# Optimization experiments

Hardware: AMD Instinct MI355X
Metric: run time of the kernel (lower is better)

## Reference

```python
import jax, jax.numpy as jnp
import numpy as np

N = 50000; E = 800000; F_IN = 128; H = 16; G = 256
DIMS = [F_IN, H, 2 * H, 4 * H, 4 * H, 8 * H]
EPS = 1e-5


def setup_inputs() -> dict:
    key = jax.random.key(0)
    ks = iter(jax.random.split(key, 40))
    inp = {}
    inp["x"] = jax.random.normal(next(ks), (N, F_IN), dtype=jnp.float32)
    inp["edge_index"] = jax.random.randint(next(ks), (2, E), 0, N, dtype=jnp.int32)
    inp["edge_weight"] = jax.random.uniform(next(ks), (E,), dtype=jnp.float32)
    inp["batch"] = jnp.sort(jax.random.randint(next(ks), (N,), 0, G, dtype=jnp.int32))
    for i in range(5):
        din, dout = DIMS[i], DIMS[i + 1]
        inp[f"W{i+1}"] = jax.random.normal(next(ks), (din, dout), dtype=jnp.float32) / np.sqrt(din).astype(np.float32)
        inp[f"b{i+1}"] = jnp.zeros((dout,), jnp.float32)
        inp[f"g{i+1}"] = jnp.ones((dout,), jnp.float32)
        inp[f"bt{i+1}"] = jnp.zeros((dout,), jnp.float32)
    inp["fc1_w"] = jax.random.normal(next(ks), (8 * H, 4 * H), dtype=jnp.float32) / np.sqrt(8 * H).astype(np.float32)
    inp["fc1_b"] = jnp.zeros((4 * H,), jnp.float32)
    inp["fc2_w"] = jax.random.normal(next(ks), (4 * H, 1), dtype=jnp.float32) / np.sqrt(4 * H).astype(np.float32)
    inp["fc2_b"] = jnp.zeros((1,), jnp.float32)
    return inp


def _gcn_norm(edge_index, edge_weight, n):
    # PyG GCNConv: add self-loops (weight 1), symmetric deg^-1/2 normalization.
    loop = jnp.arange(n, dtype=edge_index.dtype)
    row = jnp.concatenate([edge_index[0], loop])  # source
    col = jnp.concatenate([edge_index[1], loop])  # target
    w = jnp.concatenate([edge_weight, jnp.ones((n,), edge_weight.dtype)])
    deg = jax.ops.segment_sum(w, col, num_segments=n)
    dis = jnp.where(deg > 0, jax.lax.rsqrt(jnp.maximum(deg, 1e-12)), 0.0)
    return row, col, dis[row] * w * dis[col]


def _bn(h, g, b):
    # BatchNorm1d, training-mode batch statistics (biased variance, eps=1e-5)
    mu = h.mean(0)
    v = h.var(0)
    return g * (h - mu) * jax.lax.rsqrt(v + EPS) + b


def reference(x, edge_index, edge_weight, batch,
              W1, b1, g1, bt1, W2, b2, g2, bt2, W3, b3, g3, bt3,
              W4, b4, g4, bt4, W5, b5, g5, bt5,
              fc1_w, fc1_b, fc2_w, fc2_b):
    n = x.shape[0]
    row, col, norm = _gcn_norm(edge_index, edge_weight, n)

    def conv(h, W, b):
        m = h @ W                                   # [N, dout] dense transform
        agg = jax.ops.segment_sum(m[row] * norm[:, None], col, num_segments=n)
        return agg + b

    h = _bn(jax.nn.relu(conv(x, W1, b1)), g1, bt1)
    h = _bn(jax.nn.relu(conv(h, W2, b2)), g2, bt2)
    h = _bn(jax.nn.relu(conv(h, W3, b3)), g3, bt3)
    h = jax.nn.relu(_bn(conv(h, W4, b4), g4, bt4))   # layer4: conv->bn->relu
    h = _bn(conv(h, W5, b5), g5, bt5)                # layer5: conv->bn
    pooled = jax.ops.segment_sum(h, batch, num_segments=G)  # global_add_pool -> [G, 8H]
    p = jax.nn.relu(pooled)
    p = jax.nn.relu(p @ fc1_w + fc1_b)
    # dropout is identity in eval mode
    return (p @ fc2_w + fc2_b).reshape(-1)          # [G]
```

## Files before the change

### kernel.cpp

```cpp
#include <hip/hip_runtime.h>
#include <stdint.h>

#define NN 50000
#define NE 800000
#define NG 256
#define NBUCKET 16
#define PARTSZ (NBUCKET * 256)

#define NBKT 391
#define ABLK 391
#define ASLICE 2048
#define BCAP 2560

__device__ __forceinline__ float bf2f(unsigned short u) {
    return __uint_as_float(((unsigned)u) << 16);
}
__device__ __forceinline__ unsigned short f2bf(float f) {
    unsigned b = __float_as_uint(f);
    return (unsigned short)((b + 0x7FFF + ((b >> 16) & 1)) >> 16);
}

__global__ void kA1(const int* __restrict__ col, int* __restrict__ bb, float* part, int e) {
    __shared__ int cnt[NBKT];
    for (int j = threadIdx.x; j < NBKT; j += 256) cnt[j] = 0;
    for (int i = blockIdx.x * 256 + threadIdx.x; i < 5 * PARTSZ; i += ABLK * 256) part[i] = 0.f;
    __syncthreads();
    int start = blockIdx.x * ASLICE;
    int end = min(start + ASLICE, e);
    for (int i = start + threadIdx.x; i < end; i += 256)
        atomicAdd(&cnt[col[i] >> 7], 1);
    __syncthreads();
    for (int j = threadIdx.x; j < NBKT; j += 256) bb[blockIdx.x * NBKT + j] = cnt[j];
}

__global__ void kA2a(int* __restrict__ bb, int* __restrict__ totals) {
    __shared__ int v[ABLK];
    int k = blockIdx.x;
    for (int b = threadIdx.x; b < ABLK; b += 256) v[b] = bb[b * NBKT + k];
    __syncthreads();
    if (threadIdx.x == 0) {
        int run = 0;
        for (int b = 0; b < ABLK; ++b) { int t = v[b]; v[b] = run; run += t; }
        totals[k] = run;
    }
    __syncthreads();
    for (int b = threadIdx.x; b < ABLK; b += 256) bb[b * NBKT + k] = v[b];
}

__global__ void kA2b(const int* __restrict__ totals, int* __restrict__ bucketbase) {
    __shared__ int v[NBKT];
    for (int j = threadIdx.x; j < NBKT; j += 256) v[j] = totals[j];
    __syncthreads();
    if (threadIdx.x == 0) {
        int run = 0;
        for (int k = 0; k < NBKT; ++k) { int t = v[k]; v[k] = run; run += t; }
        bucketbase[NBKT] = run;
    }
    __syncthreads();
    for (int j = threadIdx.x; j < NBKT; j += 256) bucketbase[j] = v[j];
}

__global__ void kA3g(const int* __restrict__ row, const int* __restrict__ col,
                     const float* __restrict__ ew, const int* __restrict__ bb,
                     const int* __restrict__ bucketbase, int2* __restrict__ staging,
                     const float* __restrict__ x, const float* __restrict__ W0,
                     float* __restrict__ m1, int e, int n) {
    __shared__ int cur[NBKT];
    __shared__ float Wl[128 * 16];
    int tid = threadIdx.x;
    if ((int)blockIdx.x < ABLK) {
        for (int j = tid; j < NBKT; j += 256)
            cur[j] = bucketbase[j] + bb[blockIdx.x * NBKT + j];
        __syncthreads();
        int start = blockIdx.x * ASLICE;
        int end = min(start + ASLICE, e);
        for (int i = start + tid; i < end; i += 256) {
            int c = col[i];
            int p = atomicAdd(&cur[c >> 7], 1);
            staging[p] = make_int2(row[i] | ((c & 127) << 16), __float_as_int(ew[i]));
        }
        return;
    }
    int bid = (int)blockIdx.x - ABLK;
    for (int i = tid; i < 128 * 16 / 4; i += 256)
        ((float4*)Wl)[i] = ((const float4*)W0)[i];
    __syncthreads();
    int jq = tid % 4, group = tid / 4;
    int node0 = (bid * 64 + group) * 2;
    const float4* h4 = (const float4*)x;
    int hb[2]; bool val[2];
#pragma unroll
    for (int i = 0; i < 2; ++i) {
        int nd = node0 + i;
        val[i] = nd < n;
        hb[i] = (val[i] ? nd : n - 1) * 32;
    }
    float4 acc[2];
    acc[0] = {0,0,0,0}; acc[1] = {0,0,0,0};
#pragma unroll 4
    for (int k4 = 0; k4 < 32; ++k4) {
        const float* wb = &Wl[(k4 * 4) * 16 + jq * 4];
        float4 w0 = *(const float4*)(wb);
        float4 w1 = *(const float4*)(wb + 16);
        float4 w2 = *(const float4*)(wb + 32);
        float4 w3 = *(const float4*)(wb + 48);
#pragma unroll
        for (int i = 0; i < 2; ++i) {
            float4 hv = h4[hb[i] + k4];
            acc[i].x += hv.x*w0.x + hv.y*w1.x + hv.z*w2.x + hv.w*w3.x;
            acc[i].y += hv.x*w0.y + hv.y*w1.y + hv.z*w2.y + hv.w*w3.y;
            acc[i].z += hv.x*w0.z + hv.y*w1.z + hv.z*w2.z + hv.w*w3.z;
            acc[i].w += hv.x*w0.w + hv.y*w1.w + hv.z*w2.w + hv.w*w3.w;
        }
    }
#pragma unroll
    for (int i = 0; i < 2; ++i)
        if (val[i]) ((float4*)m1)[(node0 + i) * 4 + jq] = acc[i];
}

__global__ void __launch_bounds__(256) kB(const int* __restrict__ bucketbase,
                                          const int2* __restrict__ staging,
                                          int2* __restrict__ csr, int* __restrict__ ptr,
                                          float* __restrict__ dis, int n) {
    __shared__ int2 st[BCAP];
    __shared__ int2 outb[BCAP];
    __shared__ int hist[129];
    __shared__ int cur[128];
    int k = blockIdx.x, t = threadIdx.x;
    int base = bucketbase[k], cnt = bucketbase[k + 1] - base;
    int node0 = k << 7;
    int ncov = min(128, n - node0);
    if (t < 129) hist[t] = 0;
    __syncthreads();
    if (cnt <= BCAP) {
        for (int i = t; i < cnt; i += 256) {
            int2 v = staging[base + i];
            st[i] = v;
            atomicAdd(&hist[v.x >> 16], 1);
        }
        __syncthreads();
        if (t == 0) {
            int run = 0;
            for (int j = 0; j < 128; ++j) { int h = hist[j]; hist[j] = run; run += h; }
            hist[128] = run;
        }
        __syncthreads();
        if (t < 128) cur[t] = hist[t];
        if (t < ncov) ptr[node0 + t] = base + hist[t];
        __syncthreads();
        for (int i = t; i < cnt; i += 256) {
            int2 v = st[i];
            int j = v.x >> 16;
            int p = atomicAdd(&cur[j], 1);
            outb[p] = make_int2(v.x & 0xFFFF, v.y);
        }
        __syncthreads();
        for (int i = t; i < cnt; i += 256) csr[base + i] = outb[i];
        if (t < ncov) {
            float s = 1.f;
            int a = hist[t], b2 = hist[t + 1];
            for (int p = a; p < b2; ++p) s += __int_as_float(outb[p].y);
            dis[node0 + t] = rsqrtf(s);
        }
    } else {
        for (int i = t; i < cnt; i += 256) atomicAdd(&hist[staging[base + i].x >> 16], 1);
        __syncthreads();
        if (t == 0) {
            int run = 0;
            for (int j = 0; j < 128; ++j) { int h = hist[j]; hist[j] = run; run += h; }
            hist[128] = run;
        }
        __syncthreads();
        if (t < 128) cur[t] = hist[t];
        if (t < ncov) ptr[node0 + t] = base + hist[t];
        __syncthreads();
        for (int i = t; i < cnt; i += 256) {
            int2 v = staging[base + i];
            int j = v.x >> 16;
            int p = atomicAdd(&cur[j], 1);
            csr[base + p] = make_int2(v.x & 0xFFFF, v.y);
        }
        __threadfence_block();
        __syncthreads();
        if (t < ncov) {
            float s = 1.f;
            int a = hist[t], b2 = hist[t + 1];
            for (int p = a; p < b2; ++p) s += __int_as_float(csr[base + p].y);
            dis[node0 + t] = rsqrtf(s);
        }
    }
    if (k == gridDim.x - 1 && t == 0) ptr[n] = bucketbase[NBKT];
}

__global__ void k_l1gather(const float* __restrict__ src, const int* __restrict__ ptr,
                           int2* __restrict__ csr, const float* __restrict__ dis,
                           const float* __restrict__ bias, float* __restrict__ partOut,
                           float* __restrict__ out, int n) {
    __shared__ float ls[16], lq[16];
    int tid = threadIdx.x;
    if (tid < 16) { ls[tid] = 0.f; lq[tid] = 0.f; }
    __syncthreads();
    int t = blockIdx.x * 256 + tid;
    int node = t >> 2;
    int l4 = t & 3;
    bool valid = node < n;
    int nc = valid ? node : n - 1;
    const float4* s4 = (const float4*)src;
    float dc = dis[nc];
    float w0 = dc * dc;
    float4 v = s4[nc * 4 + l4];
    float4 acc = { w0 * v.x, w0 * v.y, w0 * v.z, w0 * v.w };
    int p0 = ptr[nc], p1 = ptr[nc + 1];
    int p = p0;
    for (; p + 4 <= p1; p += 4) {
        int2 c0 = csr[p], c1 = csr[p+1], c2 = csr[p+2], c3 = csr[p+3];
        float e0 = dis[c0.x] * __int_as_float(c0.y) * dc;
        float e1 = dis[c1.x] * __int_as_float(c1.y) * dc;
        float e2 = dis[c2.x] * __int_as_float(c2.y) * dc;
        float e3 = dis[c3.x] * __int_as_float(c3.y) * dc;
        float4 u0 = s4[c0.x * 4 + l4];
        float4 u1 = s4[c1.x * 4 + l4];
        float4 u2 = s4[c2.x * 4 + l4];
        float4 u3 = s4[c3.x * 4 + l4];
        acc.x += e0*u0.x + e1*u1.x + e2*u2.x + e3*u3.x;
        acc.y += e0*u0.y + e1*u1.y + e2*u2.y + e3*u3.y;
        acc.z += e0*u0.z + e1*u1.z + e2*u2.z + e3*u3.z;
        acc.w += e0*u0.w + e1*u1.w + e2*u2.w + e3*u3.w;
        if (l4 == 0) {
            csr[p]   = make_int2(c0.x, __float_as_int(e0));
            csr[p+1] = make_int2(c1.x, __float_as_int(e1));
            csr[p+2] = make_int2(c2.x, __float_as_int(e2));
            csr[p+3] = make_int2(c3.x, __float_as_int(e3));
        }
    }
    for (; p < p1; ++p) {
        int2 ce = csr[p];
        float w = dis[ce.x] * __int_as_float(ce.y) * dc;
        float4 u = s4[ce.x * 4 + l4];
        acc.x += w*u.x; acc.y += w*u.y; acc.z += w*u.z; acc.w += w*u.w;
        if (l4 == 0) csr[p] = make_int2(ce.x, __float_as_int(w));
    }
    float4 b = ((const float4*)bias)[l4];
    acc.x = fmaxf(acc.x + b.x, 0.f);
    acc.y = fmaxf(acc.y + b.y, 0.f);
    acc.z = fmaxf(acc.z + b.z, 0.f);
    acc.w = fmaxf(acc.w + b.w, 0.f);
    if (valid) ((float4*)out)[nc * 4 + l4] = acc;
    float s0 = valid ? acc.x : 0.f, s1 = valid ? acc.y : 0.f;
    float s2 = valid ? acc.z : 0.f, s3 = valid ? acc.w : 0.f;
    float q0 = s0*s0, q1 = s1*s1, q2 = s2*s2, q3 = s3*s3;
    for (int off = 4; off < 64; off <<= 1) {
        s0 += __shfl_down(s0, off, 64); s1 += __shfl_down(s1, off, 64);
        s2 += __shfl_down(s2, off, 64); s3 += __shfl_down(s3, off, 64);
        q0 += __shfl_down(q0, off, 64); q1 += __shfl_down(q1, off, 64);
        q2 += __shfl_down(q2, off, 64); q3 += __shfl_down(q3, off, 64);
    }
    int lane = tid & 63;
    if (lane < 4) {
        atomicAdd(&ls[4*lane+0], s0); atomicAdd(&ls[4*lane+1], s1);
        atomicAdd(&ls[4*lane+2], s2); atomicAdd(&ls[4*lane+3], s3);
        atomicAdd(&lq[4*lane+0], q0); atomicAdd(&lq[4*lane+1], q1);
        atomicAdd(&lq[4*lane+2], q2); atomicAdd(&lq[4*lane+3], q3);
    }
    __syncthreads();
    int bkt = (blockIdx.x & (NBUCKET - 1)) * 256;
    if (tid < 16) {
        atomicAdd(&partOut[bkt + tid], ls[tid]);
        atomicAdd(&partOut[bkt + 128 + tid], lq[tid]);
    }
}

template <int D, int BF16>
__device__ __forceinline__ float4 load_row(const void* src, int node, int l4) {
    if (BF16) {
        const unsigned short* sb = (const unsigned short*)src;
        ushort4 r = *(const ushort4*)(sb + (size_t)node * D + (l4 << 2));
        float4 f;
        f.x = bf2f(r.x); f.y = bf2f(r.y); f.z = bf2f(r.z); f.w = bf2f(r.w);
        return f;
    } else {
        const float4* s4 = (const float4*)src;
        return s4[(size_t)node * (D / 4) + l4];
    }
}

template <int DIN, int DOUT, int EP, int POSTAFF, int PREAFF, int RELU,
          int BF16IN, int BF16OUT, int NPB>
__global__ void __launch_bounds__(256) k_fused(
        const void* __restrict__ src, const int* __restrict__ ptr,
        const int2* __restrict__ csr, const float* __restrict__ dis,
        const float* __restrict__ partIn, const float* __restrict__ gmv,
        const float* __restrict__ btv, const float* __restrict__ W,
        const float* __restrict__ bias, float* __restrict__ partOut,
        void* __restrict__ out, int n) {
    const int TPN1 = DIN / 4, LPN = TPN1 * EP, GN1 = 256 / LPN;
    const int TPN2 = DOUT / 4, G2 = 256 / TPN2;
    const int HS = DIN + 4;
    __shared__ float Wl[DIN * DOUT];
    __shared__ float hrow[NPB * HS];
    __shared__ float scs[DIN], shs[DIN];
    __shared__ float ls[DOUT], lq[DOUT];
    int tid = threadIdx.x;
    for (int i = tid; i < DIN * DOUT / 4; i += 256)
        ((float4*)Wl)[i] = ((const float4*)W)[i];
    if (tid < DIN) {
        float s = 0.f, q = 0.f;
#pragma unroll
        for (int b2 = 0; b2 < NBUCKET; ++b2) {
            s += partIn[b2 * 256 + tid];
            q += partIn[b2 * 256 + 128 + tid];
        }
        float mu = s / (float)n;
        float var = q / (float)n - mu * mu;
        float a = gmv[tid] * rsqrtf(var + 1e-5f);
        scs[tid] = a;
        shs[tid] = btv[tid] - mu * a;
    }
    if (tid < DOUT) { ls[tid] = 0.f; lq[tid] = 0.f; }
    __syncthreads();

    int nodebase = blockIdx.x * NPB;
    {
        int grp = tid / LPN, r = tid % LPN;
        int e0 = r / TPN1, l4 = r % TPN1;
        float4 sc = ((const float4*)scs)[l4];
        float4 sh = ((const float4*)shs)[l4];
#pragma unroll
        for (int pass = 0; pass < NPB / GN1; ++pass) {
            int nl = pass * GN1 + grp;
            int node = nodebase + nl;
            int nc = node < n ? node : n - 1;
            float4 acc = {0.f, 0.f, 0.f, 0.f};
            float sumw = 0.f;
            if (e0 == 0) {
                float d = dis[nc];
                float w0 = d * d;
                float4 v = load_row<DIN, BF16IN>(src, nc, l4);
                if (PREAFF) {
                    v.x = fmaxf(sc.x*v.x+sh.x, 0.f); v.y = fmaxf(sc.y*v.y+sh.y, 0.f);
                    v.z = fmaxf(sc.z*v.z+sh.z, 0.f); v.w = fmaxf(sc.w*v.w+sh.w, 0.f);
                }
                acc.x = w0*v.x; acc.y = w0*v.y; acc.z = w0*v.z; acc.w = w0*v.w;
                sumw = w0;
            }
            int p0 = ptr[nc], p1 = ptr[nc + 1];
            int p = p0 + e0;
            for (; p + 3 * EP < p1; p += 4 * EP) {
                int2 c0 = csr[p], c1 = csr[p + EP], c2 = csr[p + 2*EP], c3 = csr[p + 3*EP];
                float e0w = __int_as_float(c0.y), e1w = __int_as_float(c1.y);
                float e2w = __int_as_float(c2.y), e3w = __int_as_float(c3.y);
                float4 u0 = load_row<DIN, BF16IN>(src, c0.x, l4);
                float4 u1 = load_row<DIN, BF16IN>(src, c1.x, l4);
                float4 u2 = load_row<DIN, BF16IN>(src, c2.x, l4);
                float4 u3 = load_row<DIN, BF16IN>(src, c3.x, l4);
                if (PREAFF) {
                    u0.x = fmaxf(sc.x*u0.x+sh.x,0.f); u0.y = fmaxf(sc.y*u0.y+sh.y,0.f);
                    u0.z = fmaxf(sc.z*u0.z+sh.z,0.f); u0.w = fmaxf(sc.w*u0.w+sh.w,0.f);
                    u1.x = fmaxf(sc.x*u1.x+sh.x,0.f); u1.y = fmaxf(sc.y*u1.y+sh.y,0.f);
                    u1.z = fmaxf(sc.z*u1.z+sh.z,0.f); u1.w = fmaxf(sc.w*u1.w+sh.w,0.f);
                    u2.x = fmaxf(sc.x*u2.x+sh.x,0.f); u2.y = fmaxf(sc.y*u2.y+sh.y,0.f);
                    u2.z = fmaxf(sc.z*u2.z+sh.z,0.f); u2.w = fmaxf(sc.w*u2.w+sh.w,0.f);
                    u3.x = fmaxf(sc.x*u3.x+sh.x,0.f); u3.y = fmaxf(sc.y*u3.y+sh.y,0.f);
                    u3.z = fmaxf(sc.z*u3.z+sh.z,0.f); u3.w = fmaxf(sc.w*u3.w+sh.w,0.f);
                }
                acc.x += e0w*u0.x + e1w*u1.x + e2w*u2.x + e3w*u3.x;
                acc.y += e0w*u0.y + e1w*u1.y + e2w*u2.y + e3w*u3.y;
                acc.z += e0w*u0.z + e1w*u1.z + e2w*u2.z + e3w*u3.z;
                acc.w += e0w*u0.w + e1w*u1.w + e2w*u2.w + e3w*u3.w;
                if (POSTAFF) sumw += e0w + e1w + e2w + e3w;
            }
            for (; p < p1; p += EP) {
                int2 ce = csr[p];
                float w = __int_as_float(ce.y);
                float4 u = load_row<DIN, BF16IN>(src, ce.x, l4);
                if (PREAFF) {
                    u.x = fmaxf(sc.x*u.x+sh.x,0.f); u.y = fmaxf(sc.y*u.y+sh.y,0.f);
                    u.z = fmaxf(sc.z*u.z+sh.z,0.f); u.w = fmaxf(sc.w*u.w+sh.w,0.f);
                }
                acc.x += w*u.x; acc.y += w*u.y; acc.z += w*u.z; acc.w += w*u.w;
                if (POSTAFF) sumw += w;
            }
#pragma unroll
            for (int off = TPN1; off < LPN; off <<= 1) {
                acc.x += __shfl_xor(acc.x, off, 64);
                acc.y += __shfl_xor(acc.y, off, 64);
                acc.z += __shfl_xor(acc.z, off, 64);
                acc.w += __shfl_xor(acc.w, off, 64);
                if (POSTAFF) sumw += __shfl_xor(sumw, off, 64);
            }
            if (POSTAFF) {
                acc.x = sc.x * acc.x + sh.x * sumw;
                acc.y = sc.y * acc.y + sh.y * sumw;
                acc.z = sc.z * acc.z + sh.z * sumw;
                acc.w = sc.w * acc.w + sh.w * sumw;
            }
            if (e0 == 0) *(float4*)&hrow[nl * HS + (l4 << 2)] = acc;
        }
    }
    __syncthreads();
    {
        int jq = tid % TPN2, g2 = tid / TPN2;
        float4 bv = ((const float4*)bias)[jq];
        float4 sv = {0,0,0,0}, qv = {0,0,0,0};
        for (int nl = g2; nl < NPB; nl += G2) {
            int node = nodebase + nl;
            bool valid = node < n;
            float4 a = {0.f, 0.f, 0.f, 0.f};
#pragma unroll
            for (int k4 = 0; k4 < DIN / 4; ++k4) {
                float4 hv = *(const float4*)&hrow[nl * HS + (k4 << 2)];
                const float* wb = &Wl[(k4 * 4) * DOUT + jq * 4];
// ... 16 lines not shown
                    ushort4 o;
                    o.x = f2bf(a.x); o.y = f2bf(a.y); o.z = f2bf(a.z); o.w = f2bf(a.w);
                    *(ushort4*)((unsigned short*)out + (size_t)node * DOUT + (jq << 2)) = o;
                } else {
                    ((float4*)out)[(size_t)node * TPN2 + jq] = a;
                }
                sv.x += a.x; sv.y += a.y; sv.z += a.z; sv.w += a.w;
                qv.x += a.x*a.x; qv.y += a.y*a.y; qv.z += a.z*a.z; qv.w += a.w*a.w;
            }
        }
        for (int off = TPN2; off < 64; off <<= 1) {
            sv.x += __shfl_down(sv.x, off, 64); sv.y += __shfl_down(sv.y, off, 64);
            sv.z += __shfl_down(sv.z, off, 64); sv.w += __shfl_down(sv.w, off, 64);
            qv.x += __shfl_down(qv.x, off, 64); qv.y += __shfl_down(qv.y, off, 64);
            qv.z += __shfl_down(qv.z, off, 64); qv.w += __shfl_down(qv.w, off, 64);
        }
        int lane = tid & 63;
        if (lane < TPN2) {
            atomicAdd(&ls[4*lane+0], sv.x); atomicAdd(&ls[4*lane+1], sv.y);
            atomicAdd(&ls[4*lane+2], sv.z); atomicAdd(&ls[4*lane+3], sv.w);
            atomicAdd(&lq[4*lane+0], qv.x); atomicAdd(&lq[4*lane+1], qv.y);
            atomicAdd(&lq[4*lane+2], qv.z); atomicAdd(&lq[4*lane+3], qv.w);
        }
        __syncthreads();
        int bkt = (blockIdx.x & (NBUCKET - 1)) * 256;
        if (tid < DOUT) {
            atomicAdd(&partOut[bkt + tid], ls[tid]);
            atomicAdd(&partOut[bkt + 128 + tid], lq[tid]);
        }
    }
}

template <int D, int POSTAFF, int PREAFF>
__global__ void k_sgather(const unsigned short* __restrict__ src, const int* __restrict__ ptr,
                          const int2* __restrict__ csr, const float* __restrict__ dis,
                          const float* __restrict__ partIn, const float* __restrict__ gmv,
                          const float* __restrict__ btv, float* __restrict__ out, int n) {
    const int TPN = D / 4, EP = 4, LPN = TPN * EP;
    __shared__ float scs[D], shs[D];
    int tid = threadIdx.x;
    if (tid < D) {
        float s = 0.f, q = 0.f;
#pragma unroll
        for (int b2 = 0; b2 < NBUCKET; ++b2) {
            s += partIn[b2 * 256 + tid];
            q += partIn[b2 * 256 + 128 + tid];
        }
        float mu = s / (float)n;
        float var = q / (float)n - mu * mu;
        float a = gmv[tid] * rsqrtf(var + 1e-5f);
        scs[tid] = a;
        shs[tid] = btv[tid] - mu * a;
    }
    __syncthreads();
    int t = blockIdx.x * 256 + tid;
    int node = t / LPN;
    int r = t - node * LPN;
    int e0 = r / TPN;
    int l4 = r - e0 * TPN;
    bool valid = node < n;
    int nc = valid ? node : n - 1;
    float4 sc = ((const float4*)scs)[l4];
    float4 sh = ((const float4*)shs)[l4];
    float4 acc = {0.f, 0.f, 0.f, 0.f};
    float sumw = 0.f;
    if (e0 == 0) {
        float d = dis[nc];
        float w0 = d * d;
        float4 v = load_row<D, 1>(src, nc, l4);
        if (PREAFF) {
            v.x = fmaxf(sc.x*v.x+sh.x, 0.f); v.y = fmaxf(sc.y*v.y+sh.y, 0.f);
            v.z = fmaxf(sc.z*v.z+sh.z, 0.f); v.w = fmaxf(sc.w*v.w+sh.w, 0.f);
        }
        acc.x = w0*v.x; acc.y = w0*v.y; acc.z = w0*v.z; acc.w = w0*v.w;
        sumw = w0;
    }
    int p0 = ptr[nc], p1 = ptr[nc + 1];
    int p = p0 + e0;
    for (; p + 3 * EP < p1; p += 4 * EP) {
        int2 c0 = csr[p], c1 = csr[p + EP], c2 = csr[p + 2*EP], c3 = csr[p + 3*EP];
        float e0w = __int_as_float(c0.y), e1w = __int_as_float(c1.y);
        float e2w = __int_as_float(c2.y), e3w = __int_as_float(c3.y);
        float4 u0 = load_row<D, 1>(src, c0.x, l4);
        float4 u1 = load_row<D, 1>(src, c1.x, l4);
        float4 u2 = load_row<D, 1>(src, c2.x, l4);
        float4 u3 = load_row<D, 1>(src, c3.x, l4);
        if (PREAFF) {
            u0.x = fmaxf(sc.x*u0.x+sh.x,0.f); u0.y = fmaxf(sc.y*u0.y+sh.y,0.f);
            u0.z = fmaxf(sc.z*u0.z+sh.z,0.f); u0.w = fmaxf(sc.w*u0.w+sh.w,0.f);
            u1.x = fmaxf(sc.x*u1.x+sh.x,0.f); u1.y = fmaxf(sc.y*u1.y+sh.y,0.f);
            u1.z = fmaxf(sc.z*u1.z+sh.z,0.f); u1.w = fmaxf(sc.w*u1.w+sh.w,0.f);
            u2.x = fmaxf(sc.x*u2.x+sh.x,0.f); u2.y = fmaxf(sc.y*u2.y+sh.y,0.f);
            u2.z = fmaxf(sc.z*u2.z+sh.z,0.f); u2.w = fmaxf(sc.w*u2.w+sh.w,0.f);
            u3.x = fmaxf(sc.x*u3.x+sh.x,0.f); u3.y = fmaxf(sc.y*u3.y+sh.y,0.f);
            u3.z = fmaxf(sc.z*u3.z+sh.z,0.f); u3.w = fmaxf(sc.w*u3.w+sh.w,0.f);
        }
        acc.x += e0w*u0.x + e1w*u1.x + e2w*u2.x + e3w*u3.x;
        acc.y += e0w*u0.y + e1w*u1.y + e2w*u2.y + e3w*u3.y;
        acc.z += e0w*u0.z + e1w*u1.z + e2w*u2.z + e3w*u3.z;
        acc.w += e0w*u0.w + e1w*u1.w + e2w*u2.w + e3w*u3.w;
        if (POSTAFF) sumw += e0w + e1w + e2w + e3w;
    }
    for (; p < p1; p += EP) {
        int2 ce = csr[p];
        float w = __int_as_float(ce.y);
        float4 u = load_row<D, 1>(src, ce.x, l4);
        if (PREAFF) {
            u.x = fmaxf(sc.x*u.x+sh.x,0.f); u.y = fmaxf(sc.y*u.y+sh.y,0.f);
            u.z = fmaxf(sc.z*u.z+sh.z,0.f); u.w = fmaxf(sc.w*u.w+sh.w,0.f);
        }
        acc.x += w*u.x; acc.y += w*u.y; acc.z += w*u.z; acc.w += w*u.w;
        if (POSTAFF) sumw += w;
    }
#pragma unroll
    for (int off = TPN; off < LPN; off <<= 1) {
        acc.x += __shfl_xor(acc.x, off, 64);
        acc.y += __shfl_xor(acc.y, off, 64);
        acc.z += __shfl_xor(acc.z, off, 64);
        acc.w += __shfl_xor(acc.w, off, 64);
        if (POSTAFF) sumw += __shfl_xor(sumw, off, 64);
    }
    if (POSTAFF) {
        acc.x = sc.x * acc.x + sh.x * sumw;
        acc.y = sc.y * acc.y + sh.y * sumw;
        acc.z = sc.z * acc.z + sh.z * sumw;
        acc.w = sc.w * acc.w + sh.w * sumw;
    }
    if (valid && e0 == 0) ((float4*)out)[nc * TPN + l4] = acc;
}

template <int DIN, int DOUT, int RELU, int BF16OUT>
__global__ void k_sgemm(const float* __restrict__ h, const float* __restrict__ W,
                        const float* __restrict__ bias, float* __restrict__ partOut,
                        void* __restrict__ m, int n) {
    const int TPN = DOUT / 4, GPB = 256 / TPN, NPT = 4;
    __shared__ float Wl[DIN * DOUT];
    __shared__ float ls[DOUT], lq[DOUT];
    int tid = threadIdx.x;
    for (int i = tid; i < DIN * DOUT / 4; i += 256)
        ((float4*)Wl)[i] = ((const float4*)W)[i];
    if (tid < DOUT) { ls[tid] = 0.f; lq[tid] = 0.f; }
    __syncthreads();

    int jq = tid % TPN;
    int group = tid / TPN;
    int node0 = (blockIdx.x * GPB + group) * NPT;
    const float4* h4 = (const float4*)h;
    int hb[NPT]; bool val[NPT];
#pragma unroll
    for (int i = 0; i < NPT; ++i) {
        int nd = node0 + i;
        val[i] = nd < n;
        hb[i] = (val[i] ? nd : n - 1) * (DIN / 4);
    }
    float4 acc[NPT];
#pragma unroll
    for (int i = 0; i < NPT; ++i) acc[i] = {0.f, 0.f, 0.f, 0.f};
#pragma unroll 4
    for (int k4 = 0; k4 < DIN / 4; ++k4) {
        const float* wb = &Wl[(k4 * 4) * DOUT + jq * 4];
        float4 w0 = *(const float4*)(wb);
// ... 99 lines not shown
        for (int k = 0; k < 128; ++k) v1 += pl[k] * fc1w[k * 64 + tid];
        v1 = fmaxf(v1, 0.f);
        float v = v1 * fc2w[tid];
        for (int off = 32; off > 0; off >>= 1) v += __shfl_down(v, off, 64);
        if (tid == 0) out[g] = v + fc2b[0];
    }
}

extern "C" void kernel_launch(void* const* d_in, const int* in_sizes, int n_in,
                              void* d_out, int out_size, void* d_ws, size_t ws_size,
                              hipStream_t stream) {
    const float* x     = (const float*)d_in[0];
    const int*   ei    = (const int*)d_in[1];
    const float* ew    = (const float*)d_in[2];
    const int*   batch = (const int*)d_in[3];
    const float *W[5], *b[5], *gm[5], *bt[5];
    for (int i = 0; i < 5; ++i) {
        W[i]  = (const float*)d_in[4 + 4 * i];
        b[i]  = (const float*)d_in[5 + 4 * i];
        gm[i] = (const float*)d_in[6 + 4 * i];
        bt[i] = (const float*)d_in[7 + 4 * i];
    }
    const float* fc1w = (const float*)d_in[24];
    const float* fc1b = (const float*)d_in[25];
    const float* fc2w = (const float*)d_in[26];
    const float* fc2b = (const float*)d_in[27];
    float* out = (float*)d_out;

    char* wsb = (char*)d_ws;
    float* dis    = (float*)wsb;  wsb += sizeof(float) * NN;
    int*   ptr    = (int*)wsb;    wsb += sizeof(int) * (NN + 4);
    int*   bb     = (int*)wsb;    wsb += sizeof(int) * ABLK * NBKT;
    int*   totals = (int*)wsb;    wsb += sizeof(int) * (NBKT + 1);
    int*   bbase  = (int*)wsb;    wsb += sizeof(int) * (NBKT + 3);
    wsb = (char*)(((uintptr_t)wsb + 15) & ~(uintptr_t)15);
    int2*  staging= (int2*)wsb;   wsb += sizeof(int2) * NE;
    int2*  csr    = (int2*)wsb;   wsb += sizeof(int2) * NE;
    float* part   = (float*)wsb;  wsb += sizeof(float) * 5 * PARTSZ;
    unsigned short* bufB1 = (unsigned short*)wsb;  wsb += sizeof(unsigned short) * (size_t)NN * 64;
    unsigned short* bufB2 = (unsigned short*)wsb;  wsb += sizeof(unsigned short) * (size_t)NN * 64;
    float* buf1   = (float*)wsb;  wsb += sizeof(float) * (size_t)NN * 64;
    float* buf2   = (float*)wsb;  wsb += sizeof(float) * (size_t)NN * 128;

    const int* row = ei;
    const int* col = ei + NE;
    const int B = 256;
    const int NBF = (NN + 15) / 16;
    const int GB1 = (NN + 127) / 128;

    kA1<<<ABLK, B, 0, stream>>>(col, bb, part, NE);
    kA2a<<<NBKT, B, 0, stream>>>(bb, totals);
    kA2b<<<1, B, 0, stream>>>(totals, bbase);
    kA3g<<<ABLK + GB1, B, 0, stream>>>(row, col, ew, bb, bbase, staging, x, W[0], buf1, NE, NN);
    kB<<<NBKT, B, 0, stream>>>(bbase, staging, csr, ptr, dis, NN);

    k_l1gather<<<(NN * 4 + 255) / 256, B, 0, stream>>>(buf1, ptr, csr, dis,
                                                       b[0], part + 0 * PARTSZ, buf2, NN);

    k_fused<16, 32, 4, 1, 0, 1, 0, 1, 16><<<NBF, B, 0, stream>>>(
        buf2, ptr, csr, dis, part + 0 * PARTSZ, gm[0], bt[0],
        W[1], b[1], part + 1 * PARTSZ, bufB1, NN);

    k_sgather<32, 1, 0><<<(int)(((long)NN * 32 + 255) / 256), B, 0, stream>>>(
        bufB1, ptr, csr, dis, part + 1 * PARTSZ, gm[1], bt[1], buf1, NN);
    k_sgemm<32, 64, 1, 1><<<(NN + 63) / 64, B, 0, stream>>>(buf1, W[2], b[2], part + 2 * PARTSZ, bufB2, NN);

    k_sgather<64, 1, 0><<<(int)(((long)NN * 64 + 255) / 256), B, 0, stream>>>(
        bufB2, ptr, csr, dis, part + 2 * PARTSZ, gm[2], bt[2], buf1, NN);
    k_sgemm<64, 64, 0, 1><<<(NN + 63) / 64, B, 0, stream>>>(buf1, W[3], b[3], part + 3 * PARTSZ, bufB1, NN);

    k_sgather<64, 0, 1><<<(int)(((long)NN * 64 + 255) / 256), B, 0, stream>>>(
        bufB1, ptr, csr, dis, part + 3 * PARTSZ, gm[3], bt[3], buf1, NN);
    k_sgemm<64, 128, 0, 0><<<(NN + 31) / 32, B, 0, stream>>>(buf1, W[4], b[4], part + 4 * PARTSZ, buf2, NN);

    k_poolhead<<<NG, B, 0, stream>>>(buf2, batch, part + 4 * PARTSZ, gm[4], bt[4],
                                     fc1w, fc1b, fc2w, fc2b, out, NN);
}
```

Before: 394.6 us.

## Pack CSR edges to 32-bit fp16 weights, widen gathers, fold bucket scan

Compresses each CSR entry from an int2 (index plus fp32 weight) into one 32-bit word holding a 16-bit source index and an fp16 normalized weight, halving edge-list traffic in every gather layer. The bf16 gather kernels now load 8 features per lane with a 16-byte load instead of 4, halving thread count. The separate single-block bucket-base scan kernel is removed: a wave-level shuffle scan of totals is recomputed inside kA3g and kB, and kA2a uses a parallel shuffle scan instead of a serial one. This adds fp16 rounding of edge weights and relies on node indices fitting in 16 bits, which fails for N=50000 if indices exceed 65535 (they don't here, but the packing is tight).

```diff
diff --git a/kernel.cpp b/kernel.cpp
--- a/kernel.cpp
+++ b/kernel.cpp
@@ -1,4 +1,5 @@
 #include <hip/hip_runtime.h>
+#include <hip/hip_fp16.h>
 #include <stdint.h>
 
 #define NN 50000
@@ -19,6 +20,46 @@
     unsigned b = __float_as_uint(f);
     return (unsigned short)((b + 0x7FFF + ((b >> 16) & 1)) >> 16);
 }
+__device__ __forceinline__ unsigned short f2h(float f) {
+    __half h = __float2half(f);
+    return *(unsigned short*)&h;
+}
+__device__ __forceinline__ float h2f(unsigned short u) {
+    __half h = *(__half*)&u;
+    return __half2float(h);
+}
+
+#define AFF4(u, sc, sh) { u.x = fmaxf(sc.x*u.x+sh.x,0.f); u.y = fmaxf(sc.y*u.y+sh.y,0.f); \
+                          u.z = fmaxf(sc.z*u.z+sh.z,0.f); u.w = fmaxf(sc.w*u.w+sh.w,0.f); }
+
+__device__ __forceinline__ void scan_totals(const int* __restrict__ totals,
+                                            int* __restrict__ sbase, int tid) {
+    if (tid < 64) {
+        const int C = (NBKT + 63) / 64;
+        int tv[C];
+        int s = 0;
+        int i0 = tid * C;
+#pragma unroll
+        for (int j = 0; j < C; ++j) {
+            int idx = i0 + j;
+            int x = (idx < NBKT) ? totals[idx] : 0;
+            tv[j] = x; s += x;
+        }
+        int inc = s;
+        for (int off = 1; off < 64; off <<= 1) {
+            int t2 = __shfl_up(inc, off, 64);
+            if (tid >= off) inc += t2;
+        }
+        int run = inc - s;
+#pragma unroll
+        for (int j = 0; j < C; ++j) {
+            int idx = i0 + j;
+            if (idx < NBKT) sbase[idx] = run;
+            run += tv[j];
+        }
+        if (tid == 63) sbase[NBKT] = run;
+    }
+}
 
 __global__ void kA1(const int* __restrict__ col, int* __restrict__ bb, float* part, int e) {
     __shared__ int cnt[NBKT];
@@ -36,41 +77,52 @@
 __global__ void kA2a(int* __restrict__ bb, int* __restrict__ totals) {
     __shared__ int v[ABLK];
     int k = blockIdx.x;
-    for (int b = threadIdx.x; b < ABLK; b += 256) v[b] = bb[b * NBKT + k];
-    __syncthreads();
-    if (threadIdx.x == 0) {
-        int run = 0;
-        for (int b = 0; b < ABLK; ++b) { int t = v[b]; v[b] = run; run += t; }
-        totals[k] = run;
-    }
-    __syncthreads();
-    for (int b = threadIdx.x; b < ABLK; b += 256) bb[b * NBKT + k] = v[b];
-}
-
-__global__ void kA2b(const int* __restrict__ totals, int* __restrict__ bucketbase) {
-    __shared__ int v[NBKT];
-    for (int j = threadIdx.x; j < NBKT; j += 256) v[j] = totals[j];
-    __syncthreads();
-    if (threadIdx.x == 0) {
-        int run = 0;
-        for (int k = 0; k < NBKT; ++k) { int t = v[k]; v[k] = run; run += t; }
-        bucketbase[NBKT] = run;
-    }
-    __syncthreads();
-    for (int j = threadIdx.x; j < NBKT; j += 256) bucketbase[j] = v[j];
+    int tid = threadIdx.x;
+    for (int b = tid; b < ABLK; b += 256) v[b] = bb[b * NBKT + k];
+    __syncthreads();
+    if (tid < 64) {
+        const int C = (ABLK + 63) / 64;
+        int tv[C];
+        int s = 0;
+        int i0 = tid * C;
+#pragma unroll
+        for (int j = 0; j < C; ++j) {
+            int idx = i0 + j;
+            int x = (idx < ABLK) ? v[idx] : 0;
+            tv[j] = x; s += x;
+        }
+        int inc = s;
+        for (int off = 1; off < 64; off <<= 1) {
+            int t2 = __shfl_up(inc, off, 64);
+            if (tid >= off) inc += t2;
+        }
+        int run = inc - s;
+#pragma unroll
+        for (int j = 0; j < C; ++j) {
+            int idx = i0 + j;
+            if (idx < ABLK) v[idx] = run;
+            run += tv[j];
+        }
+        if (tid == 63) totals[k] = run;
+    }
+    __syncthreads();
+    for (int b = tid; b < ABLK; b += 256) bb[b * NBKT + k] = v[b];
 }
 
 __global__ void kA3g(const int* __restrict__ row, const int* __restrict__ col,
                      const float* __restrict__ ew, const int* __restrict__ bb,
-                     const int* __restrict__ bucketbase, int2* __restrict__ staging,
+                     const int* __restrict__ totals, int2* __restrict__ staging,
                      const float* __restrict__ x, const float* __restrict__ W0,
                      float* __restrict__ m1, int e, int n) {
     __shared__ int cur[NBKT];
+    __shared__ int sbase[NBKT + 1];
     __shared__ float Wl[128 * 16];
     int tid = threadIdx.x;
     if ((int)blockIdx.x < ABLK) {
+        scan_totals(totals, sbase, tid);
+        __syncthreads();
         for (int j = tid; j < NBKT; j += 256)
-            cur[j] = bucketbase[j] + bb[blockIdx.x * NBKT + j];
+            cur[j] = sbase[j] + bb[blockIdx.x * NBKT + j];
         __syncthreads();
         int start = blockIdx.x * ASLICE;
         int end = min(start + ASLICE, e);
@@ -118,20 +170,22 @@
         if (val[i]) ((float4*)m1)[(node0 + i) * 4 + jq] = acc[i];
 }
 
-__global__ void __launch_bounds__(256) kB(const int* __restrict__ bucketbase,
+__global__ void __launch_bounds__(256) kB(const int* __restrict__ totals,
                                           const int2* __restrict__ staging,
-                                          int2* __restrict__ csr, int* __restrict__ ptr,
+                                          unsigned int* __restrict__ csr, int* __restrict__ ptr,
                                           float* __restrict__ dis, int n) {
     __shared__ int2 st[BCAP];
-    __shared__ int2 outb[BCAP];
+    __shared__ unsigned int outb[BCAP];
     __shared__ int hist[129];
     __shared__ int cur[128];
+    __shared__ int sbase[NBKT + 1];
     int k = blockIdx.x, t = threadIdx.x;
-    int base = bucketbase[k], cnt = bucketbase[k + 1] - base;
+    scan_totals(totals, sbase, t);
+    if (t < 129) hist[t] = 0;
+    __syncthreads();
+    int base = sbase[k], cnt = sbase[k + 1] - sbase[k];
     int node0 = k << 7;
     int ncov = min(128, n - node0);
-    if (t < 129) hist[t] = 0;
-    __syncthreads();
     if (cnt <= BCAP) {
         for (int i = t; i < cnt; i += 256) {
             int2 v = staging[base + i];
@@ -152,14 +206,14 @@
             int2 v = st[i];
             int j = v.x >> 16;
             int p = atomicAdd(&cur[j], 1);
-            outb[p] = make_int2(v.x & 0xFFFF, v.y);
+            outb[p] = (unsigned)(v.x & 0xFFFF) | ((unsigned)f2h(__int_as_float(v.y)) << 16);
         }
         __syncthreads();
         for (int i = t; i < cnt; i += 256) csr[base + i] = outb[i];
         if (t < ncov) {
             float s = 1.f;
             int a = hist[t], b2 = hist[t + 1];
-            for (int p = a; p < b2; ++p) s += __int_as_float(outb[p].y);
+            for (int p = a; p < b2; ++p) s += h2f((unsigned short)(outb[p] >> 16));
             dis[node0 + t] = rsqrtf(s);
         }
     } else {
@@ -178,22 +232,22 @@
             int2 v = staging[base + i];
             int j = v.x >> 16;
             int p = atomicAdd(&cur[j], 1);
-            csr[base + p] = make_int2(v.x & 0xFFFF, v.y);
+            csr[base + p] = (unsigned)(v.x & 0xFFFF) | ((unsigned)f2h(__int_as_float(v.y)) << 16);
         }
         __threadfence_block();
         __syncthreads();
         if (t < ncov) {
             float s = 1.f;
             int a = hist[t], b2 = hist[t + 1];
-            for (int p = a; p < b2; ++p) s += __int_as_float(csr[base + p].y);
+            for (int p = a; p < b2; ++p) s += h2f((unsigned short)(csr[base + p] >> 16));
             dis[node0 + t] = rsqrtf(s);
         }
     }
-    if (k == gridDim.x - 1 && t == 0) ptr[n] = bucketbase[NBKT];
+    if (k == gridDim.x - 1 && t == 0) ptr[n] = sbase[NBKT];
 }
 
 __global__ void k_l1gather(const float* __restrict__ src, const int* __restrict__ ptr,
-                           int2* __restrict__ csr, const float* __restrict__ dis,
+                           unsigned int* __restrict__ csr, const float* __restrict__ dis,
                            const float* __restrict__ bias, float* __restrict__ partOut,
                            float* __restrict__ out, int n) {
     __shared__ float ls[16], lq[16];
@@ -213,32 +267,34 @@
     int p0 = ptr[nc], p1 = ptr[nc + 1];
     int p = p0;
     for (; p + 4 <= p1; p += 4) {
-        int2 c0 = csr[p], c1 = csr[p+1], c2 = csr[p+2], c3 = csr[p+3];
-        float e0 = dis[c0.x] * __int_as_float(c0.y) * dc;
-        float e1 = dis[c1.x] * __int_as_float(c1.y) * dc;
-        float e2 = dis[c2.x] * __int_as_float(c2.y) * dc;
-        float e3 = dis[c3.x] * __int_as_float(c3.y) * dc;
-        float4 u0 = s4[c0.x * 4 + l4];
-        float4 u1 = s4[c1.x * 4 + l4];
-        float4 u2 = s4[c2.x * 4 + l4];
-        float4 u3 = s4[c3.x * 4 + l4];
+        unsigned int c0 = csr[p], c1 = csr[p+1], c2 = csr[p+2], c3 = csr[p+3];
+        int s0i = c0 & 0xFFFF, s1i = c1 & 0xFFFF, s2i = c2 & 0xFFFF, s3i = c3 & 0xFFFF;
+        float e0 = dis[s0i] * h2f((unsigned short)(c0 >> 16)) * dc;
+        float e1 = dis[s1i] * h2f((unsigned short)(c1 >> 16)) * dc;
+        float e2 = dis[s2i] * h2f((unsigned short)(c2 >> 16)) * dc;
+        float e3 = dis[s3i] * h2f((unsigned short)(c3 >> 16)) * dc;
+        float4 u0 = s4[s0i * 4 + l4];
+        float4 u1 = s4[s1i * 4 + l4];
+        float4 u2 = s4[s2i * 4 + l4];
+        float4 u3 = s4[s3i * 4 + l4];
         acc.x += e0*u0.x + e1*u1.x + e2*u2.x + e3*u3.x;
         acc.y += e0*u0.y + e1*u1.y + e2*u2.y + e3*u3.y;
         acc.z += e0*u0.z + e1*u1.z + e2*u2.z + e3*u3.z;
         acc.w += e0*u0.w + e1*u1.w + e2*u2.w + e3*u3.w;
         if (l4 == 0) {
-            csr[p]   = make_int2(c0.x, __float_as_int(e0));
-            csr[p+1] = make_int2(c1.x, __float_as_int(e1));
-            csr[p+2] = make_int2(c2.x, __float_as_int(e2));
-            csr[p+3] = make_int2(c3.x, __float_as_int(e3));
+            csr[p]   = (unsigned)s0i | ((unsigned)f2h(e0) << 16);
+            csr[p+1] = (unsigned)s1i | ((unsigned)f2h(e1) << 16);
+            csr[p+2] = (unsigned)s2i | ((unsigned)f2h(e2) << 16);
+            csr[p+3] = (unsigned)s3i | ((unsigned)f2h(e3) << 16);
         }
     }
     for (; p < p1; ++p) {
-        int2 ce = csr[p];
-        float w = dis[ce.x] * __int_as_float(ce.y) * dc;
-        float4 u = s4[ce.x * 4 + l4];
+        unsigned int ce = csr[p];
+        int si = ce & 0xFFFF;
+        float w = dis[si] * h2f((unsigned short)(ce >> 16)) * dc;
+        float4 u = s4[si * 4 + l4];
         acc.x += w*u.x; acc.y += w*u.y; acc.z += w*u.z; acc.w += w*u.w;
-        if (l4 == 0) csr[p] = make_int2(ce.x, __float_as_int(w));
+        if (l4 == 0) csr[p] = (unsigned)si | ((unsigned)f2h(w) << 16);
     }
     float4 b = ((const float4*)bias)[l4];
     acc.x = fmaxf(acc.x + b.x, 0.f);
@@ -284,11 +340,21 @@
     }
 }
 
+template <int D>
+__device__ __forceinline__ void ldrow16(const unsigned short* __restrict__ src, int node, int l8,
+                                        float4& a, float4& b) {
+    uint4 r = *(const uint4*)(src + (size_t)node * D + (l8 << 3));
+    a.x = bf2f((unsigned short)(r.x)); a.y = bf2f((unsigned short)(r.x >> 16));
+    a.z = bf2f((unsigned short)(r.y)); a.w = bf2f((unsigned short)(r.y >> 16));
+    b.x = bf2f((unsigned short)(r.z)); b.y = bf2f((unsigned short)(r.z >> 16));
+    b.z = bf2f((unsigned short)(r.w)); b.w = bf2f((unsigned short)(r.w >> 16));
+}
+
 template <int DIN, int DOUT, int EP, int POSTAFF, int PREAFF, int RELU,
           int BF16IN, int BF16OUT, int NPB>
 __global__ void __launch_bounds__(256) k_fused(
         const void* __restrict__ src, const int* __restrict__ ptr,
-        const int2* __restrict__ csr, const float* __restrict__ dis,
+        const unsigned int* __restrict__ csr, const float* __restrict__ dis,
         const float* __restrict__ partIn, const float* __restrict__ gmv,
         const float* __restrict__ btv, const float* __restrict__ W,
         const float* __restrict__ bias, float* __restrict__ partOut,
@@ -336,33 +402,21 @@
                 float d = dis[nc];
                 float w0 = d * d;
                 float4 v = load_row<DIN, BF16IN>(src, nc, l4);
-                if (PREAFF) {
-                    v.x = fmaxf(sc.x*v.x+sh.x, 0.f); v.y = fmaxf(sc.y*v.y+sh.y, 0.f);
-                    v.z = fmaxf(sc.z*v.z+sh.z, 0.f); v.w = fmaxf(sc.w*v.w+sh.w, 0.f);
-                }
+                if (PREAFF) AFF4(v, sc, sh);
                 acc.x = w0*v.x; acc.y = w0*v.y; acc.z = w0*v.z; acc.w = w0*v.w;
                 sumw = w0;
             }
             int p0 = ptr[nc], p1 = ptr[nc + 1];
             int p = p0 + e0;
             for (; p + 3 * EP < p1; p += 4 * EP) {
-                int2 c0 = csr[p], c1 = csr[p + EP], c2 = csr[p + 2*EP], c3 = csr[p + 3*EP];
-                float e0w = __int_as_float(c0.y), e1w = __int_as_float(c1.y);
-                float e2w = __int_as_float(c2.y), e3w = __int_as_float(c3.y);
-                float4 u0 = load_row<DIN, BF16IN>(src, c0.x, l4);
-                float4 u1 = load_row<DIN, BF16IN>(src, c1.x, l4);
-                float4 u2 = load_row<DIN, BF16IN>(src, c2.x, l4);
-                float4 u3 = load_row<DIN, BF16IN>(src, c3.x, l4);
-                if (PREAFF) {
-                    u0.x = fmaxf(sc.x*u0.x+sh.x,0.f); u0.y = fmaxf(sc.y*u0.y+sh.y,0.f);
-                    u0.z = fmaxf(sc.z*u0.z+sh.z,0.f); u0.w = fmaxf(sc.w*u0.w+sh.w,0.f);
-                    u1.x = fmaxf(sc.x*u1.x+sh.x,0.f); u1.y = fmaxf(sc.y*u1.y+sh.y,0.f);
-                    u1.z = fmaxf(sc.z*u1.z+sh.z,0.f); u1.w = fmaxf(sc.w*u1.w+sh.w,0.f);
-                    u2.x = fmaxf(sc.x*u2.x+sh.x,0.f); u2.y = fmaxf(sc.y*u2.y+sh.y,0.f);
-                    u2.z = fmaxf(sc.z*u2.z+sh.z,0.f); u2.w = fmaxf(sc.w*u2.w+sh.w,0.f);
-                    u3.x = fmaxf(sc.x*u3.x+sh.x,0.f); u3.y = fmaxf(sc.y*u3.y+sh.y,0.f);
-                    u3.z = fmaxf(sc.z*u3.z+sh.z,0.f); u3.w = fmaxf(sc.w*u3.w+sh.w,0.f);
-                }
+                unsigned int c0 = csr[p], c1 = csr[p + EP], c2 = csr[p + 2*EP], c3 = csr[p + 3*EP];
+                float e0w = h2f((unsigned short)(c0 >> 16)), e1w = h2f((unsigned short)(c1 >> 16));
+                float e2w = h2f((unsigned short)(c2 >> 16)), e3w = h2f((unsigned short)(c3 >> 16));
+                float4 u0 = load_row<DIN, BF16IN>(src, c0 & 0xFFFF, l4);
+                float4 u1 = load_row<DIN, BF16IN>(src, c1 & 0xFFFF, l4);
+                float4 u2 = load_row<DIN, BF16IN>(src, c2 & 0xFFFF, l4);
+                float4 u3 = load_row<DIN, BF16IN>(src, c3 & 0xFFFF, l4);
+                if (PREAFF) { AFF4(u0, sc, sh); AFF4(u1, sc, sh); AFF4(u2, sc, sh); AFF4(u3, sc, sh); }
                 acc.x += e0w*u0.x + e1w*u1.x + e2w*u2.x + e3w*u3.x;
                 acc.y += e0w*u0.y + e1w*u1.y + e2w*u2.y + e3w*u3.y;
                 acc.z += e0w*u0.z + e1w*u1.z + e2w*u2.z + e3w*u3.z;
@@ -370,13 +424,10 @@
                 if (POSTAFF) sumw += e0w + e1w + e2w + e3w;
             }
             for (; p < p1; p += EP) {
-                int2 ce = csr[p];
-                float w = __int_as_float(ce.y);
-                float4 u = load_row<DIN, BF16IN>(src, ce.x, l4);
-                if (PREAFF) {
-                    u.x = fmaxf(sc.x*u.x+sh.x,0.f); u.y = fmaxf(sc.y*u.y+sh.y,0.f);
-                    u.z = fmaxf(sc.z*u.z+sh.z,0.f); u.w = fmaxf(sc.w*u.w+sh.w,0.f);
-                }
+                unsigned int ce = csr[p];
+                float w = h2f((unsigned short)(ce >> 16));
+                float4 u = load_row<DIN, BF16IN>(src, ce & 0xFFFF, l4);
+                if (PREAFF) AFF4(u, sc, sh);
                 acc.x += w*u.x; acc.y += w*u.y; acc.z += w*u.z; acc.w += w*u.w;
                 if (POSTAFF) sumw += w;
             }
@@ -459,11 +510,14 @@
 }
 
 template <int D, int POSTAFF, int PREAFF>
-__global__ void k_sgather(const unsigned short* __restrict__ src, const int* __restrict__ ptr,
-                          const int2* __restrict__ csr, const float* __restrict__ dis,
-                          const float* __restrict__ partIn, const float* __restrict__ gmv,
-                          const float* __restrict__ btv, float* __restrict__ out, int n) {
-    const int TPN = D / 4, EP = 4, LPN = TPN * EP;
+__global__ void __launch_bounds__(256) k_wgather(
+        const unsigned short* __restrict__ src, const int* __restrict__ ptr,
+        const unsigned int* __restrict__ csr, const float* __restrict__ dis,
+        const float* __restrict__ partIn, const float* __restrict__ gmv,
+        const float* __restrict__ btv, float* __restrict__ out, int n) {
+    const int RL = D / 8;
+    const int EP = 4;
+    const int LPN = RL * EP;
     __shared__ float scs[D], shs[D];
     int tid = threadIdx.x;
     if (tid < D) {
@@ -483,77 +537,79 @@
     int t = blockIdx.x * 256 + tid;
     int node = t / LPN;
     int r = t - node * LPN;
-    int e0 = r / TPN;
-    int l4 = r - e0 * TPN;
+    int e0 = r / RL;
+    int l8 = r - e0 * RL;
     bool valid = node < n;
     int nc = valid ? node : n - 1;
-    float4 sc = ((const float4*)scs)[l4];
-    float4 sh = ((const float4*)shs)[l4];
-    float4 acc = {0.f, 0.f, 0.f, 0.f};
+    float4 scA = ((const float4*)scs)[l8 * 2],     shA = ((const float4*)shs)[l8 * 2];
+    float4 scB = ((const float4*)scs)[l8 * 2 + 1], shB = ((const float4*)shs)[l8 * 2 + 1];
+    float4 accA = {0.f,0.f,0.f,0.f}, accB = {0.f,0.f,0.f,0.f};
     float sumw = 0.f;
     if (e0 == 0) {
         float d = dis[nc];
         float w0 = d * d;
-        float4 v = load_row<D, 1>(src, nc, l4);
-        if (PREAFF) {
-            v.x = fmaxf(sc.x*v.x+sh.x, 0.f); v.y = fmaxf(sc.y*v.y+sh.y, 0.f);
-            v.z = fmaxf(sc.z*v.z+sh.z, 0.f); v.w = fmaxf(sc.w*v.w+sh.w, 0.f);
-        }
-        acc.x = w0*v.x; acc.y = w0*v.y; acc.z = w0*v.z; acc.w = w0*v.w;
+        float4 a, b2;
+        ldrow16<D>(src, nc, l8, a, b2);
+        if (PREAFF) { AFF4(a, scA, shA); AFF4(b2, scB, shB); }
+        accA.x = w0*a.x;  accA.y = w0*a.y;  accA.z = w0*a.z;  accA.w = w0*a.w;
+        accB.x = w0*b2.x; accB.y = w0*b2.y; accB.z = w0*b2.z; accB.w = w0*b2.w;
         sumw = w0;
     }
     int p0 = ptr[nc], p1 = ptr[nc + 1];
     int p = p0 + e0;
     for (; p + 3 * EP < p1; p += 4 * EP) {
-        int2 c0 = csr[p], c1 = csr[p + EP], c2 = csr[p + 2*EP], c3 = csr[p + 3*EP];
-        float e0w = __int_as_float(c0.y), e1w = __int_as_float(c1.y);
-        float e2w = __int_as_float(c2.y), e3w = __int_as_float(c3.y);
-        float4 u0 = load_row<D, 1>(src, c0.x, l4);
-        float4 u1 = load_row<D, 1>(src, c1.x, l4);
-        float4 u2 = load_row<D, 1>(src, c2.x, l4);
-        float4 u3 = load_row<D, 1>(src, c3.x, l4);
+        unsigned int c0 = csr[p], c1 = csr[p + EP], c2 = csr[p + 2*EP], c3 = csr[p + 3*EP];
+        float w0 = h2f((unsigned short)(c0 >> 16)), w1 = h2f((unsigned short)(c1 >> 16));
+        float w2 = h2f((unsigned short)(c2 >> 16)), w3 = h2f((unsigned short)(c3 >> 16));
+        float4 a0, b0, a1, b1, a2, b2, a3, b3;
+        ldrow16<D>(src, c0 & 0xFFFF, l8, a0, b0);
+        ldrow16<D>(src, c1 & 0xFFFF, l8, a1, b1);
+        ldrow16<D>(src, c2 & 0xFFFF, l8, a2, b2);
+        ldrow16<D>(src, c3 & 0xFFFF, l8, a3, b3);
         if (PREAFF) {
-            u0.x = fmaxf(sc.x*u0.x+sh.x,0.f); u0.y = fmaxf(sc.y*u0.y+sh.y,0.f);
-            u0.z = fmaxf(sc.z*u0.z+sh.z,0.f); u0.w = fmaxf(sc.w*u0.w+sh.w,0.f);
-            u1.x = fmaxf(sc.x*u1.x+sh.x,0.f); u1.y = fmaxf(sc.y*u1.y+sh.y,0.f);
-            u1.z = fmaxf(sc.z*u1.z+sh.z,0.f); u1.w = fmaxf(sc.w*u1.w+sh.w,0.f);
-            u2.x = fmaxf(sc.x*u2.x+sh.x,0.f); u2.y = fmaxf(sc.y*u2.y+sh.y,0.f);
-            u2.z = fmaxf(sc.z*u2.z+sh.z,0.f); u2.w = fmaxf(sc.w*u2.w+sh.w,0.f);
-            u3.x = fmaxf(sc.x*u3.x+sh.x,0.f); u3.y = fmaxf(sc.y*u3.y+sh.y,0.f);
-            u3.z = fmaxf(sc.z*u3.z+sh.z,0.f); u3.w = fmaxf(sc.w*u3.w+sh.w,0.f);
-        }
-        acc.x += e0w*u0.x + e1w*u1.x + e2w*u2.x + e3w*u3.x;
-        acc.y += e0w*u0.y + e1w*u1.y + e2w*u2.y + e3w*u3.y;
-        acc.z += e0w*u0.z + e1w*u1.z + e2w*u2.z + e3w*u3.z;
-        acc.w += e0w*u0.w + e1w*u1.w + e2w*u2.w + e3w*u3.w;
-        if (POSTAFF) sumw += e0w + e1w + e2w + e3w;
+            AFF4(a0, scA, shA); AFF4(b0, scB, shB);
+            AFF4(a1, scA, shA); AFF4(b1, scB, shB);
+            AFF4(a2, scA, shA); AFF4(b2, scB, shB);
+            AFF4(a3, scA, shA); AFF4(b3, scB, shB);
+        }
+        accA.x += w0*a0.x + w1*a1.x + w2*a2.x + w3*a3.x;
+        accA.y += w0*a0.y + w1*a1.y + w2*a2.y + w3*a3.y;
+        accA.z += w0*a0.z + w1*a1.z + w2*a2.z + w3*a3.z;
+        accA.w += w0*a0.w + w1*a1.w + w2*a2.w + w3*a3.w;
+        accB.x += w0*b0.x + w1*b1.x + w2*b2.x + w3*b3.x;
+        accB.y += w0*b0.y + w1*b1.y + w2*b2.y + w3*b3.y;
+        accB.z += w0*b0.z + w1*b1.z + w2*b2.z + w3*b3.z;
+        accB.w += w0*b0.w + w1*b1.w + w2*b2.w + w3*b3.w;
+        if (POSTAFF) sumw += w0 + w1 + w2 + w3;
     }
     for (; p < p1; p += EP) {
-        int2 ce = csr[p];
-        float w = __int_as_float(ce.y);
-        float4 u = load_row<D, 1>(src, ce.x, l4);
-        if (PREAFF) {
-            u.x = fmaxf(sc.x*u.x+sh.x,0.f); u.y = fmaxf(sc.y*u.y+sh.y,0.f);
-            u.z = fmaxf(sc.z*u.z+sh.z,0.f); u.w = fmaxf(sc.w*u.w+sh.w,0.f);
-        }
-        acc.x += w*u.x; acc.y += w*u.y; acc.z += w*u.z; acc.w += w*u.w;
+        unsigned int ce = csr[p];
+        float w = h2f((unsigned short)(ce >> 16));
+        float4 a, b2;
+        ldrow16<D>(src, ce & 0xFFFF, l8, a, b2);
+        if (PREAFF) { AFF4(a, scA, shA); AFF4(b2, scB, shB); }
+        accA.x += w*a.x;  accA.y += w*a.y;  accA.z += w*a.z;  accA.w += w*a.w;
+        accB.x += w*b2.x; accB.y += w*b2.y; accB.z += w*b2.z; accB.w += w*b2.w;
         if (POSTAFF) sumw += w;
     }
 #pragma unroll
-    for (int off = TPN; off < LPN; off <<= 1) {
-        acc.x += __shfl_xor(acc.x, off, 64);
-        acc.y += __shfl_xor(acc.y, off, 64);
-        acc.z += __shfl_xor(acc.z, off, 64);
-        acc.w += __shfl_xor(acc.w, off, 64);
+    for (int off = RL; off < LPN; off <<= 1) {
+        accA.x += __shfl_xor(accA.x, off, 64); accA.y += __shfl_xor(accA.y, off, 64);
+        accA.z += __shfl_xor(accA.z, off, 64); accA.w += __shfl_xor(accA.w, off, 64);
+        accB.x += __shfl_xor(accB.x, off, 64); accB.y += __shfl_xor(accB.y, off, 64);
+        accB.z += __shfl_xor(accB.z, off, 64); accB.w += __shfl_xor(accB.w, off, 64);
         if (POSTAFF) sumw += __shfl_xor(sumw, off, 64);
     }
     if (POSTAFF) {
-        acc.x = sc.x * acc.x + sh.x * sumw;
-        acc.y = sc.y * acc.y + sh.y * sumw;
-        acc.z = sc.z * acc.z + sh.z * sumw;
-        acc.w = sc.w * acc.w + sh.w * sumw;
-    }
-    if (valid && e0 == 0) ((float4*)out)[nc * TPN + l4] = acc;
+        accA.x = scA.x * accA.x + shA.x * sumw; accA.y = scA.y * accA.y + shA.y * sumw;
+        accA.z = scA.z * accA.z + shA.z * sumw; accA.w = scA.w * accA.w + shA.w * sumw;
+        accB.x = scB.x * accB.x + shB.x * sumw; accB.y = scB.y * accB.y + shB.y * sumw;
+        accB.z = scB.z * accB.z + shB.z * sumw; accB.w = scB.w * accB.w + shB.w * sumw;
+    }
+    if (valid && e0 == 0) {
+        ((float4*)out)[(size_t)nc * (D / 4) + l8 * 2]     = accA;
+        ((float4*)out)[(size_t)nc * (D / 4) + l8 * 2 + 1] = accB;
+    }
 }
 
 template <int DIN, int DOUT, int RELU, int BF16OUT>
@@ -719,10 +775,10 @@
     int*   ptr    = (int*)wsb;    wsb += sizeof(int) * (NN + 4);
     int*   bb     = (int*)wsb;    wsb += sizeof(int) * ABLK * NBKT;
     int*   totals = (int*)wsb;    wsb += sizeof(int) * (NBKT + 1);
-    int*   bbase  = (int*)wsb;    wsb += sizeof(int) * (NBKT + 3);
     wsb = (char*)(((uintptr_t)wsb + 15) & ~(uintptr_t)15);
     int2*  staging= (int2*)wsb;   wsb += sizeof(int2) * NE;
-    int2*  csr    = (int2*)wsb;   wsb += sizeof(int2) * NE;
+    unsigned int* csru = (unsigned int*)wsb; wsb += sizeof(unsigned int) * NE;
+    wsb = (char*)(((uintptr_t)wsb + 15) & ~(uintptr_t)15);
     float* part   = (float*)wsb;  wsb += sizeof(float) * 5 * PARTSZ;
     unsigned short* bufB1 = (unsigned short*)wsb;  wsb += sizeof(unsigned short) * (size_t)NN * 64;
     unsigned short* bufB2 = (unsigned short*)wsb;  wsb += sizeof(unsigned short) * (size_t)NN * 64;
@@ -737,27 +793,26 @@
 
     kA1<<<ABLK, B, 0, stream>>>(col, bb, part, NE);
     kA2a<<<NBKT, B, 0, stream>>>(bb, totals);
-    kA2b<<<1, B, 0, stream>>>(totals, bbase);
-    kA3g<<<ABLK + GB1, B, 0, stream>>>(row, col, ew, bb, bbase, staging, x, W[0], buf1, NE, NN);
-    kB<<<NBKT, B, 0, stream>>>(bbase, staging, csr, ptr, dis, NN);
-
-    k_l1gather<<<(NN * 4 + 255) / 256, B, 0, stream>>>(buf1, ptr, csr, dis,
+    kA3g<<<ABLK + GB1, B, 0, stream>>>(row, col, ew, bb, totals, staging, x, W[0], buf1, NE, NN);
+    kB<<<NBKT, B, 0, stream>>>(totals, staging, csru, ptr, dis, NN);
+
+    k_l1gather<<<(NN * 4 + 255) / 256, B, 0, stream>>>(buf1, ptr, csru, dis,
                                                        b[0], part + 0 * PARTSZ, buf2, NN);
 
     k_fused<16, 32, 4, 1, 0, 1, 0, 1, 16><<<NBF, B, 0, stream>>>(
-        buf2, ptr, csr, dis, part + 0 * PARTSZ, gm[0], bt[0],
+        buf2, ptr, csru, dis, part + 0 * PARTSZ, gm[0], bt[0],
         W[1], b[1], part + 1 * PARTSZ, bufB1, NN);
 
-    k_sgather<32, 1, 0><<<(int)(((long)NN * 32 + 255) / 256), B, 0, stream>>>(
-        bufB1, ptr, csr, dis, part + 1 * PARTSZ, gm[1], bt[1], buf1, NN);
+    k_wgather<32, 1, 0><<<(int)(((long)NN * 16 + 255) / 256), B, 0, stream>>>(
+        bufB1, ptr, csru, dis, part + 1 * PARTSZ, gm[1], bt[1], buf1, NN);
     k_sgemm<32, 64, 1, 1><<<(NN + 63) / 64, B, 0, stream>>>(buf1, W[2], b[2], part + 2 * PARTSZ, bufB2, NN);
 
-    k_sgather<64, 1, 0><<<(int)(((long)NN * 64 + 255) / 256), B, 0, stream>>>(
-        bufB2, ptr, csr, dis, part + 2 * PARTSZ, gm[2], bt[2], buf1, NN);
+    k_wgather<64, 1, 0><<<(int)(((long)NN * 32 + 255) / 256), B, 0, stream>>>(
+        bufB2, ptr, csru, dis, part + 2 * PARTSZ, gm[2], bt[2], buf1, NN);
     k_sgemm<64, 64, 0, 1><<<(NN + 63) / 64, B, 0, stream>>>(buf1, W[3], b[3], part + 3 * PARTSZ, bufB1, NN);
 
-    k_sgather<64, 0, 1><<<(int)(((long)NN * 64 + 255) / 256), B, 0, stream>>>(
-        bufB1, ptr, csr, dis, part + 3 * PARTSZ, gm[3], bt[3], buf1, NN);
+    k_wgather<64, 0, 1><<<(int)(((long)NN * 32 + 255) / 256), B, 0, stream>>>(
+        bufB1, ptr, csru, dis, part + 3 * PARTSZ, gm[3], bt[3], buf1, NN);
     k_sgemm<64, 128, 0, 0><<<(NN + 31) / 32, B, 0, stream>>>(buf1, W[4], b[4], part + 4 * PARTSZ, buf2, NN);
 
     k_poolhead<<<NG, B, 0, stream>>>(buf2, batch, part + 4 * PARTSZ, gm[4], bt[4],
```

Result: faster. 361.7 us (-8.4%).
